# Kernel optimization log

Hardware: AMD Instinct MI355X
Metric: run time of the kernel (lower is better)

## Reference

```python
import jax, jax.numpy as jnp
import numpy as np

B, S, D, F, E, K = 2, 2048, 1024, 4096, 8, 2


def setup_inputs() -> dict:
    key = jax.random.key(0)
    ks = jax.random.split(key, 6)
    s = 0.02  # init scale
    return {
        "x": jax.random.normal(ks[0], (B, S, D), dtype=jnp.float32),
        "Wr": jax.random.normal(ks[1], (D, E), dtype=jnp.float32) * s,
        "br": jnp.zeros((E,), dtype=jnp.float32),
        "W1": jax.random.normal(ks[2], (E, D, F), dtype=jnp.float32) * s,
        "b1": jnp.zeros((E, F), dtype=jnp.float32),
        "W2": jax.random.normal(ks[3], (E, F, D), dtype=jnp.float32) * s,
        "b2": jnp.zeros((E, D), dtype=jnp.float32),
        "top_k": K,
    }


def reference(x, Wr, br, W1, b1, W2, b2, top_k):
    b, s, d = x.shape
    e = Wr.shape[1]
    xt = x.reshape(-1, d)                              # [T, D], T = b*s
    logits = xt @ Wr + br                              # [T, E]
    probs = jax.nn.softmax(logits, axis=-1)            # [T, E] router probabilities
    topw, topi = jax.lax.top_k(probs, top_k)           # [T, K] each
    # combine weight per (token, expert): weight if expert in token's top-k else 0
    cw = jnp.sum(jax.nn.one_hot(topi, e, dtype=x.dtype) * topw[..., None], axis=1)  # [T, E]
    # dense grouped FFN: every expert over every token, then weighted combine
    h = jax.nn.relu(jnp.einsum('td,edf->tef', xt, W1) + b1)   # [T, E, F]
    y = jnp.einsum('tef,efd->ted', h, W2) + b2                # [T, E, D]
    out = jnp.einsum('te,ted->td', cw, y).reshape(b, s, d)    # [B, S, D]
    return out, probs.reshape(b, s, e)
```

## Files before the change

### kernel.cpp

```cpp
#include <hip/hip_runtime.h>
#include <hip/hip_bf16.h>


#define T_TOK 4096
#define D_DIM 1024
#define F_DIM 4096
#define E_NUM 8
#define CAP_ROWS 10240
#define N_TILES (CAP_ROWS/256)

typedef __attribute__((ext_vector_type(8))) short short8v;
typedef __attribute__((ext_vector_type(8))) unsigned short ushort8v;
typedef __attribute__((ext_vector_type(4))) float f32x4;

static __device__ __forceinline__ unsigned short f2bf(float f){
  union { float f; unsigned u; } v; v.f = f;
  unsigned r = (v.u + 0x7fffu + ((v.u >> 16) & 1u)) >> 16;
  return (unsigned short)r;
}
static __device__ __forceinline__ float bf2f(unsigned short s){
  union { unsigned u; float f; } v; v.u = ((unsigned)s) << 16;
  return v.f;
}

static __device__ __forceinline__ void gload16(const void* g, void* l) {
  __builtin_amdgcn_global_load_lds(
      (const __attribute__((address_space(1))) unsigned int*)g,
      (__attribute__((address_space(3))) unsigned int*)l, 16, 0, 0);
}

__global__ __launch_bounds__(256) void k_init(int* counts, int* cursor,
                                              int* rows_token, float* rows_w){
  const int gid = blockIdx.x * 256 + threadIdx.x;
  if (gid < E_NUM) counts[gid] = 0;
  else if (gid < 2*E_NUM) cursor[gid - E_NUM] = 0;
  if (gid < CAP_ROWS) { rows_token[gid] = 0; rows_w[gid] = 0.f; }
}

__global__ __launch_bounds__(256) void k_router(
    const float* __restrict__ x, const float* __restrict__ Wr,
    const float* __restrict__ br, float* __restrict__ probs_out,
    int* __restrict__ topi, float* __restrict__ topw, int* __restrict__ counts,
    unsigned short* __restrict__ xbf)
{
  const int lane = threadIdx.x & 63;
  const int t = blockIdx.x * 4 + (threadIdx.x >> 6);
  float xv[16];
  #pragma unroll
  for (int i = 0; i < 16; ++i) xv[i] = x[(size_t)t*D_DIM + i*64 + lane];
  #pragma unroll
  for (int i = 0; i < 16; ++i) xbf[(size_t)t*D_DIM + i*64 + lane] = f2bf(xv[i]);
  float pe[E_NUM];
  #pragma unroll
  for (int e = 0; e < E_NUM; ++e) {
    float p = 0.f;
    #pragma unroll
    for (int i = 0; i < 16; ++i) p += xv[i] * Wr[(i*64 + lane)*E_NUM + e];
    #pragma unroll
    for (int off = 32; off >= 1; off >>= 1) p += __shfl_xor(p, off);
    pe[e] = p + br[e];
  }
  float m = pe[0];
  #pragma unroll
  for (int e = 1; e < E_NUM; ++e) m = fmaxf(m, pe[e]);
  float s = 0.f;
  #pragma unroll
  for (int e = 0; e < E_NUM; ++e) { pe[e] = expf(pe[e] - m); s += pe[e]; }
  const float inv = 1.f / s;
  int e1 = 0; float v1 = pe[0];
  #pragma unroll
  for (int e = 1; e < E_NUM; ++e) if (pe[e] > v1) { v1 = pe[e]; e1 = e; }
  int e2 = (e1 == 0) ? 1 : 0; float v2 = pe[e2];
  #pragma unroll
  for (int e = 0; e < E_NUM; ++e) if (e != e1 && pe[e] > v2) { v2 = pe[e]; e2 = e; }
  if (lane == 0) {
    #pragma unroll
    for (int e = 0; e < E_NUM; ++e) probs_out[(size_t)t*E_NUM + e] = pe[e] * inv;
    topi[t*2+0] = e1; topw[t*2+0] = v1 * inv;
    topi[t*2+1] = e2; topw[t*2+1] = v2 * inv;
    atomicAdd(&counts[e1], 1);
    atomicAdd(&counts[e2], 1);
  }
}

__global__ __launch_bounds__(256) void k_scan(
    const int* __restrict__ counts, int* __restrict__ pbase,
    int* __restrict__ tile_e)
{
  __shared__ int base_s[E_NUM + 1];
  const int tid = threadIdx.x;
  if (tid == 0) {
    int base = 0;
    #pragma unroll
    for (int e = 0; e < E_NUM; ++e) {
      base_s[e] = base;
      base += ((counts[e] + 255) >> 8) << 8;
    }
    base_s[E_NUM] = base;
  }
  __syncthreads();
  if (tid <= E_NUM) pbase[tid] = base_s[tid];
  if (tid < N_TILES) {
    const int r0 = tid << 8;
    int e = -1;
    #pragma unroll
    for (int k = 0; k < E_NUM; ++k)
      if (r0 >= base_s[k] && r0 < base_s[k+1]) e = k;
    tile_e[tid] = e;
  }
}

__global__ __launch_bounds__(256) void k_assign(
    const int* __restrict__ topi, const float* __restrict__ topw,
    const int* __restrict__ pbase, int* __restrict__ cursor,
    int* __restrict__ rows_token, float* __restrict__ rows_w,
    int* __restrict__ pair_of)
{
  const int t = blockIdx.x * 256 + threadIdx.x;
  if (t < T_TOK) {
    #pragma unroll
    for (int k = 0; k < 2; ++k) {
      const int e = topi[t*2+k];
      const int slot = atomicAdd(&cursor[e], 1);
      const int pid = pbase[e] + slot;
      rows_token[pid] = t;
      rows_w[pid] = topw[t*2+k];
      pair_of[t*2+k] = pid;
    }
  }
}

template<int R, int C>
__global__ __launch_bounds__(256) void k_tcvt(const float* __restrict__ in,
                                              unsigned short* __restrict__ out)
{
  const size_t eo = (size_t)blockIdx.z * R * C;
  const int r0 = blockIdx.y * 64, c0 = blockIdx.x * 64;
  __shared__ unsigned short ls[64][66];
  const int t = threadIdx.x;
  const int rr = t >> 4, cc = (t & 15) * 4;
  #pragma unroll
  for (int p = 0; p < 4; ++p) {
    const float4 v = *(const float4*)&in[eo + (size_t)(r0 + p*16 + rr)*C + c0 + cc];
    ls[p*16+rr][cc+0]=f2bf(v.x); ls[p*16+rr][cc+1]=f2bf(v.y);
    ls[p*16+rr][cc+2]=f2bf(v.z); ls[p*16+rr][cc+3]=f2bf(v.w);
  }
  __syncthreads();
  const int kc = (t & 7) * 8, nn0 = t >> 3;
  #pragma unroll
  for (int p = 0; p < 2; ++p) {
    const int nn = nn0 + p*32;
    ushort8v o;
    #pragma unroll
    for (int j = 0; j < 8; ++j) o[j] = ls[kc + j][nn];
    *(ushort8v*)&out[eo + (size_t)(c0 + nn)*R + r0 + kc] = o;
  }
}

template<bool GATHER, int NDIM, int KFULL, int EPI>
__global__ __launch_bounds__(512, 2) void k_gemm(
    const unsigned short* __restrict__ A,
    const unsigned short* __restrict__ Bt,
    const float* __restrict__ bias,
    const int* __restrict__ tile_e,
    const int* __restrict__ rows_token,
    const float* __restrict__ rows_w,
    unsigned short* __restrict__ outp,
    int nkt, int kch)
{
  const int tot = gridDim.x * gridDim.y;
  int flat = blockIdx.x * gridDim.y + blockIdx.y;
  flat = (flat & 7) * (tot >> 3) + (flat >> 3);
  const int bx = flat / gridDim.y;
  const int by = flat % gridDim.y;
  const int e = tile_e[by];
  if (e < 0) return;
  const int rt = by * 256;
  const int ntc = bx * 256;
  const int koff = blockIdx.z * kch;
  __shared__ __align__(16) unsigned short LB[3][512*32];
  const int tid = threadIdx.x;
  const int lane = tid & 63;
  const int w = tid >> 6;
  const int lrow = lane >> 2;
  const int g = (lane & 3) ^ (lrow & 3);
  const unsigned short* gp[4];
  unsigned lbase[4];
  if (w < 4) {
    #pragma unroll
    for (int i = 0; i < 4; ++i) {
      const int rl = w*64 + i*16 + lrow;
      const int rowidx = GATHER ? rows_token[rt + rl] : (rt + rl);
      gp[i] = A + (size_t)rowidx * KFULL + koff + g*8;
      lbase[i] = (unsigned)((w*64 + i*16) * 32);
    }
  } else {
    const unsigned short* Be = Bt + (size_t)e * NDIM * KFULL;
    #pragma unroll
    for (int i = 0; i < 4; ++i) {
      const int rl = (w-4)*64 + i*16 + lrow;
      gp[i] = Be + (size_t)(ntc + rl) * KFULL + koff + g*8;
      lbase[i] = (unsigned)((256 + (w-4)*64 + i*16) * 32);
    }
  }
  const int wr = w >> 2, wc = w & 3;
  const int cl = lane & 15, rgb = lane >> 4;
  const int ch = (rgb ^ (cl & 3)) * 8;
  f32x4 acc[8][4] = {};

  #define STG(tt, ss)                                  \
    { const int _ko = (tt) * 32;                       \
      gload16(gp[0] + _ko, &LB[ss][lbase[0]]);         \
      gload16(gp[1] + _ko, &LB[ss][lbase[1]]);         \
      gload16(gp[2] + _ko, &LB[ss][lbase[2]]);         \
      gload16(gp[3] + _ko, &LB[ss][lbase[3]]); }

  STG(0, 0)
  STG(1, 1)
  asm volatile("s_waitcnt vmcnt(4)" ::: "memory");
  __builtin_amdgcn_s_barrier();

  int cur = 0;
  for (int t = 0; t < nkt; ++t) {
    const int pb = (cur == 0) ? 2 : (cur - 1);
    if (t + 2 < nkt) STG(t+2, pb)
    const unsigned short* Sb = LB[cur];
    short8v a[8], b[4];
    #pragma unroll
    for (int m = 0; m < 8; ++m)
      a[m] = *(const short8v*)&Sb[(wr*128 + m*16 + cl)*32 + ch];
    #pragma unroll
    for (int n = 0; n < 4; ++n)
      b[n] = *(const short8v*)&Sb[(256 + wc*64 + n*16 + cl)*32 + ch];
    #pragma unroll
    for (int m = 0; m < 8; ++m)
      #pragma unroll
      for (int n = 0; n < 4; ++n)
        acc[m][n] = __builtin_amdgcn_mfma_f32_16x16x32_bf16(a[m], b[n], acc[m][n], 0, 0, 0);
    if (t + 2 < nkt) { asm volatile("s_waitcnt vmcnt(4)" ::: "memory"); }
    else             { asm volatile("s_waitcnt vmcnt(0)" ::: "memory"); }
    __builtin_amdgcn_s_barrier();
    cur = (cur == 2) ? 0 : (cur + 1);
  }
  #undef STG

  unsigned short* op = outp;
  if (EPI == 2) op += (size_t)blockIdx.z * CAP_ROWS * NDIM;
  const bool addb = (EPI == 1) || (blockIdx.z == 0);
  const size_t ebias = (size_t)e * NDIM;
  #pragma unroll
  for (int m = 0; m < 8; ++m) {
    const int row = rt + wr*128 + m*16 + rgb*4;
    float4 rw4 = make_float4(0,0,0,0);
    if (EPI == 2) rw4 = *(const float4*)&rows_w[row];
    #pragma unroll
    for (int n = 0; n < 4; ++n) {
      const int col = ntc + wc*64 + n*16 + cl;
      const float bv = addb ? bias[ebias + col] : 0.f;
      #pragma unroll
      for (int r = 0; r < 4; ++r) {
        float v = acc[m][n][r] + bv;
        if (EPI == 1) v = fmaxf(v, 0.f);
        else          v *= ((const float*)&rw4)[r];
        const unsigned short hb = f2bf(v);
        const unsigned short ob = (unsigned short)__shfl_xor((int)(unsigned)hb, 1);
        if ((lane & 1) == 0) {
          const unsigned pk = (unsigned)hb | ((unsigned)ob << 16);
          *(unsigned*)&op[(size_t)(row + r)*NDIM + col] = pk;
        }
      }
    }
  }
}

__global__ __launch_bounds__(256) void k_combine(
    const unsigned short* __restrict__ yp, const int* __restrict__ pair_of,
    float* __restrict__ out, int ksplit)
{
  const int gid = blockIdx.x * 256 + threadIdx.x;
  const int t = gid >> 7;
  const int c = (gid & 127) * 8;
  float o[8] = {0,0,0,0,0,0,0,0};
  #pragma unroll
  for (int k = 0; k < 2; ++k) {
    const int p = pair_of[t*2+k];
    for (int s = 0; s < ksplit; ++s) {
      const ushort8v v = *(const ushort8v*)&yp[((size_t)s*CAP_ROWS + p)*D_DIM + c];
      #pragma unroll
      for (int j = 0; j < 8; ++j) o[j] += bf2f(v[j]);
    }
  }
  float4 o0; o0.x=o[0]; o0.y=o[1]; o0.z=o[2]; o0.w=o[3];
  float4 o1; o1.x=o[4]; o1.y=o[5]; o1.z=o[6]; o1.w=o[7];
  *(float4*)&out[(size_t)t*D_DIM + c]     = o0;
  *(float4*)&out[(size_t)t*D_DIM + c + 4] = o1;
}

extern "C" void kernel_launch(void* const* d_in, const int* in_sizes, int n_in,
                              void* d_out, int out_size, void* d_ws, size_t ws_size,
                              hipStream_t stream)
{
  const float* x  = (const float*)d_in[0];
  const float* Wr = (const float*)d_in[1];
  const float* br = (const float*)d_in[2];
  const float* W1 = (const float*)d_in[3];
  const float* b1 = (const float*)d_in[4];
  const float* W2 = (const float*)d_in[5];
  const float* b2 = (const float*)d_in[6];
  (void)in_sizes; (void)n_in; (void)out_size;

  float* out   = (float*)d_out;
  float* probs = out + (size_t)T_TOK * D_DIM;

  char* w = (char*)d_ws;
  size_t off = 0;
  int*   counts     = (int*)(w + off); off += 256;
  int*   cursor     = (int*)(w + off); off += 256;
  int*   pbase      = (int*)(w + off); off += 512;
  int*   tile_e     = (int*)(w + off); off += 3072;
  int*   topi       = (int*)(w + off); off += (size_t)T_TOK*2*4;
  float* topw       = (float*)(w + off); off += (size_t)T_TOK*2*4;
  int*   pair_of    = (int*)(w + off); off += (size_t)T_TOK*2*4;
  int*   rows_token = (int*)(w + off); off += (size_t)CAP_ROWS*4;
  float* rows_w     = (float*)(w + off); off += (size_t)CAP_ROWS*4;
  off = (off + 255) & ~(size_t)255;
  unsigned short* xbf = (unsigned short*)(w + off); off += (size_t)T_TOK*D_DIM*2;
  unsigned short* Wt  = (unsigned short*)(w + off); off += (size_t)E_NUM*D_DIM*F_DIM*2;
  unsigned short* h   = (unsigned short*)(w + off); off += (size_t)CAP_ROWS*F_DIM*2;
  unsigned short* yp  = (unsigned short*)(w + off);
  const size_t ypart_bytes = (size_t)CAP_ROWS * D_DIM * 2;
  int ksplit = 1;
  if (ws_size >= off + 4 * ypart_bytes) ksplit = 4;
  else if (ws_size >= off + 2 * ypart_bytes) ksplit = 2;
  const int kch2 = F_DIM / ksplit;
  const int nkt2 = kch2 / 32;

  k_init<<<(CAP_ROWS + 255) / 256, 256, 0, stream>>>(counts, cursor, rows_token, rows_w);
  k_router<<<T_TOK / 4, 256, 0, stream>>>(x, Wr, br, probs, topi, topw, counts, xbf);
  k_scan<<<1, 256, 0, stream>>>(counts, pbase, tile_e);
  k_assign<<<T_TOK / 256, 256, 0, stream>>>(topi, topw, pbase, cursor,
                                            rows_token, rows_w, pair_of);
  k_tcvt<D_DIM, F_DIM><<<dim3(F_DIM/64, D_DIM/64, E_NUM), 256, 0, stream>>>(W1, Wt);
  k_gemm<true, F_DIM, D_DIM, 1><<<dim3(F_DIM/256, N_TILES, 1), 512, 0, stream>>>(
      xbf, Wt, b1, tile_e, rows_token, rows_w, h, D_DIM/32, D_DIM);
  k_tcvt<F_DIM, D_DIM><<<dim3(D_DIM/64, F_DIM/64, E_NUM), 256, 0, stream>>>(W2, Wt);
  k_gemm<false, D_DIM, F_DIM, 2><<<dim3(D_DIM/256, N_TILES, ksplit), 512, 0, stream>>>(
      h, Wt, b2, tile_e, rows_token, rows_w, yp, nkt2, kch2);
  k_combine<<<T_TOK * D_DIM / 8 / 256, 256, 0, stream>>>(yp, pair_of, out, ksplit);
}
```

Before: 475.1 us.

## Restructure grouped GEMM mainloop: BK=64 double buffer with interleaved LDS reads and MFMA

Replaces the triple-buffered BK=32 mainloop with a double-buffered BK=64 tile. Each iteration is split into four MFMA sub-blocks, and LDS fragment loads for the next sub-block are interleaved with the current one. Global staging is split into two halves, issued at different points in the iteration. The change also adds a new XOR swizzle over 8 chunks and uses s_setprio around the MFMA bursts. The aim is to halve loop/barrier overhead per K and to hide LDS and global latency behind math, at the cost of many more barriers per iteration and higher register pressure.

Result: faster. 464.2 us (-2.3%).

```diff
diff --git a/kernel.cpp b/kernel.cpp
--- a/kernel.cpp
+++ b/kernel.cpp
@@ -178,71 +178,129 @@
   const int rt = by * 256;
   const int ntc = bx * 256;
   const int koff = blockIdx.z * kch;
-  __shared__ __align__(16) unsigned short LB[3][512*32];
+  __shared__ __align__(16) unsigned short LB[2][512 * 64];
   const int tid = threadIdx.x;
   const int lane = tid & 63;
   const int w = tid >> 6;
-  const int lrow = lane >> 2;
-  const int g = (lane & 3) ^ (lrow & 3);
-  const unsigned short* gp[4];
-  unsigned lbase[4];
+  const int lr = lane >> 3;
+  const int g  = (lane & 7) ^ lr;
+  const unsigned short* gp[8];
+  unsigned lbase[8];
   if (w < 4) {
     #pragma unroll
-    for (int i = 0; i < 4; ++i) {
-      const int rl = w*64 + i*16 + lrow;
+    for (int i = 0; i < 8; ++i) {
+      const int rl = w*64 + i*8 + lr;
       const int rowidx = GATHER ? rows_token[rt + rl] : (rt + rl);
       gp[i] = A + (size_t)rowidx * KFULL + koff + g*8;
-      lbase[i] = (unsigned)((w*64 + i*16) * 32);
+      lbase[i] = (unsigned)((w*64 + i*8) * 64);
     }
   } else {
     const unsigned short* Be = Bt + (size_t)e * NDIM * KFULL;
     #pragma unroll
-    for (int i = 0; i < 4; ++i) {
-      const int rl = (w-4)*64 + i*16 + lrow;
+    for (int i = 0; i < 8; ++i) {
+      const int rl = (w-4)*64 + i*8 + lr;
       gp[i] = Be + (size_t)(ntc + rl) * KFULL + koff + g*8;
-      lbase[i] = (unsigned)((256 + (w-4)*64 + i*16) * 32);
+      lbase[i] = (unsigned)((256 + (w-4)*64 + i*8) * 64);
     }
   }
   const int wr = w >> 2, wc = w & 3;
   const int cl = lane & 15, rgb = lane >> 4;
-  const int ch = (rgb ^ (cl & 3)) * 8;
+  const int sz = cl & 7;
   f32x4 acc[8][4] = {};
 
-  #define STG(tt, ss)                                  \
-    { const int _ko = (tt) * 32;                       \
-      gload16(gp[0] + _ko, &LB[ss][lbase[0]]);         \
-      gload16(gp[1] + _ko, &LB[ss][lbase[1]]);         \
-      gload16(gp[2] + _ko, &LB[ss][lbase[2]]);         \
-      gload16(gp[3] + _ko, &LB[ss][lbase[3]]); }
-
-  STG(0, 0)
-  STG(1, 1)
+  #define STG4(tt, bb, c0)                                    \
+    { const int _ko = (tt) * 64;                              \
+      gload16(gp[c0+0] + _ko, &LB[bb][lbase[c0+0]]);          \
+      gload16(gp[c0+1] + _ko, &LB[bb][lbase[c0+1]]);          \
+      gload16(gp[c0+2] + _ko, &LB[bb][lbase[c0+2]]);          \
+      gload16(gp[c0+3] + _ko, &LB[bb][lbase[c0+3]]); }
+  #define LGK0  asm volatile("s_waitcnt lgkmcnt(0)" ::: "memory")
+  #define BAR   __builtin_amdgcn_s_barrier()
+
+  STG4(0, 0, 0) STG4(0, 0, 4)
+  STG4(1, 1, 0)
   asm volatile("s_waitcnt vmcnt(4)" ::: "memory");
-  __builtin_amdgcn_s_barrier();
-
-  int cur = 0;
+  BAR;
+
   for (int t = 0; t < nkt; ++t) {
-    const int pb = (cur == 0) ? 2 : (cur - 1);
-    if (t + 2 < nkt) STG(t+2, pb)
-    const unsigned short* Sb = LB[cur];
-    short8v a[8], b[4];
-    #pragma unroll
-    for (int m = 0; m < 8; ++m)
-      a[m] = *(const short8v*)&Sb[(wr*128 + m*16 + cl)*32 + ch];
-    #pragma unroll
-    for (int n = 0; n < 4; ++n)
-      b[n] = *(const short8v*)&Sb[(256 + wc*64 + n*16 + cl)*32 + ch];
-    #pragma unroll
-    for (int m = 0; m < 8; ++m)
-      #pragma unroll
-      for (int n = 0; n < 4; ++n)
-        acc[m][n] = __builtin_amdgcn_mfma_f32_16x16x32_bf16(a[m], b[n], acc[m][n], 0, 0, 0);
-    if (t + 2 < nkt) { asm volatile("s_waitcnt vmcnt(4)" ::: "memory"); }
-    else             { asm volatile("s_waitcnt vmcnt(0)" ::: "memory"); }
-    __builtin_amdgcn_s_barrier();
-    cur = (cur == 2) ? 0 : (cur + 1);
-  }
-  #undef STG
+    const int bb = t & 1;
+    const unsigned short* Sb = &LB[bb][0];
+    short8v a[4][2], b[4][2];
+    #pragma unroll
+    for (int m = 0; m < 4; ++m) {
+      a[m][0] = *(const short8v*)&Sb[(wr*128 + m*16 + cl)*64 + ((0*4+rgb)^sz)*8];
+      a[m][1] = *(const short8v*)&Sb[(wr*128 + m*16 + cl)*64 + ((1*4+rgb)^sz)*8];
+    }
+    #pragma unroll
+    for (int n = 0; n < 2; ++n) {
+      b[n][0] = *(const short8v*)&Sb[(256 + wc*64 + n*16 + cl)*64 + ((0*4+rgb)^sz)*8];
+      b[n][1] = *(const short8v*)&Sb[(256 + wc*64 + n*16 + cl)*64 + ((1*4+rgb)^sz)*8];
+    }
+    if (t + 1 < nkt) STG4(t+1, bb^1, 4)
+    BAR; LGK0;
+    __builtin_amdgcn_s_setprio(1);
+    #pragma unroll
+    for (int m = 0; m < 4; ++m)
+      #pragma unroll
+      for (int n = 0; n < 2; ++n) {
+        acc[m][n] = __builtin_amdgcn_mfma_f32_16x16x32_bf16(a[m][0], b[n][0], acc[m][n], 0, 0, 0);
+        acc[m][n] = __builtin_amdgcn_mfma_f32_16x16x32_bf16(a[m][1], b[n][1], acc[m][n], 0, 0, 0);
+      }
+    __builtin_amdgcn_s_setprio(0);
+    BAR;
+    #pragma unroll
+    for (int n = 2; n < 4; ++n) {
+      b[n][0] = *(const short8v*)&Sb[(256 + wc*64 + n*16 + cl)*64 + ((0*4+rgb)^sz)*8];
+      b[n][1] = *(const short8v*)&Sb[(256 + wc*64 + n*16 + cl)*64 + ((1*4+rgb)^sz)*8];
+    }
+    BAR; LGK0;
+    __builtin_amdgcn_s_setprio(1);
+    #pragma unroll
+    for (int m = 0; m < 4; ++m)
+      #pragma unroll
+      for (int n = 2; n < 4; ++n) {
+        acc[m][n] = __builtin_amdgcn_mfma_f32_16x16x32_bf16(a[m][0], b[n][0], acc[m][n], 0, 0, 0);
+        acc[m][n] = __builtin_amdgcn_mfma_f32_16x16x32_bf16(a[m][1], b[n][1], acc[m][n], 0, 0, 0);
+      }
+    __builtin_amdgcn_s_setprio(0);
+    BAR;
+    #pragma unroll
+    for (int m = 0; m < 4; ++m) {
+      a[m][0] = *(const short8v*)&Sb[(wr*128 + (m+4)*16 + cl)*64 + ((0*4+rgb)^sz)*8];
+      a[m][1] = *(const short8v*)&Sb[(wr*128 + (m+4)*16 + cl)*64 + ((1*4+rgb)^sz)*8];
+    }
+    BAR; LGK0;
+    __builtin_amdgcn_s_setprio(1);
+    #pragma unroll
+    for (int m = 0; m < 4; ++m)
+      #pragma unroll
+      for (int n = 0; n < 2; ++n) {
+        acc[m+4][n] = __builtin_amdgcn_mfma_f32_16x16x32_bf16(a[m][0], b[n][0], acc[m+4][n], 0, 0, 0);
+        acc[m+4][n] = __builtin_amdgcn_mfma_f32_16x16x32_bf16(a[m][1], b[n][1], acc[m+4][n], 0, 0, 0);
+      }
+    __builtin_amdgcn_s_setprio(0);
+    BAR;
+    if (t + 2 < nkt) {
+      STG4(t+2, bb, 0)
+      asm volatile("s_waitcnt vmcnt(4)" ::: "memory");
+    } else if (t + 1 < nkt) {
+      asm volatile("s_waitcnt vmcnt(0)" ::: "memory");
+    }
+    BAR;
+    __builtin_amdgcn_s_setprio(1);
+    #pragma unroll
+    for (int m = 0; m < 4; ++m)
+      #pragma unroll
+      for (int n = 2; n < 4; ++n) {
+        acc[m+4][n] = __builtin_amdgcn_mfma_f32_16x16x32_bf16(a[m][0], b[n][0], acc[m+4][n], 0, 0, 0);
+        acc[m+4][n] = __builtin_amdgcn_mfma_f32_16x16x32_bf16(a[m][1], b[n][1], acc[m+4][n], 0, 0, 0);
+      }
+    __builtin_amdgcn_s_setprio(0);
+    BAR;
+  }
+  #undef STG4
+  #undef LGK0
+  #undef BAR
 
   unsigned short* op = outp;
   if (EPI == 2) op += (size_t)blockIdx.z * CAP_ROWS * NDIM;
@@ -333,7 +391,7 @@
   if (ws_size >= off + 4 * ypart_bytes) ksplit = 4;
   else if (ws_size >= off + 2 * ypart_bytes) ksplit = 2;
   const int kch2 = F_DIM / ksplit;
-  const int nkt2 = kch2 / 32;
+  const int nkt2 = kch2 / 64;
 
   k_init<<<(CAP_ROWS + 255) / 256, 256, 0, stream>>>(counts, cursor, rows_token, rows_w);
   k_router<<<T_TOK / 4, 256, 0, stream>>>(x, Wr, br, probs, topi, topw, counts, xbf);
@@ -342,7 +400,7 @@
                                             rows_token, rows_w, pair_of);
   k_tcvt<D_DIM, F_DIM><<<dim3(F_DIM/64, D_DIM/64, E_NUM), 256, 0, stream>>>(W1, Wt);
   k_gemm<true, F_DIM, D_DIM, 1><<<dim3(F_DIM/256, N_TILES, 1), 512, 0, stream>>>(
-      xbf, Wt, b1, tile_e, rows_token, rows_w, h, D_DIM/32, D_DIM);
+      xbf, Wt, b1, tile_e, rows_token, rows_w, h, D_DIM/64, D_DIM);
   k_tcvt<F_DIM, D_DIM><<<dim3(D_DIM/64, F_DIM/64, E_NUM), 256, 0, stream>>>(W2, Wt);
   k_gemm<false, D_DIM, F_DIM, 2><<<dim3(D_DIM/256, N_TILES, ksplit), 512, 0, stream>>>(
       h, Wt, b2, tile_e, rows_token, rows_w, yp, nkt2, kch2);
```

## Shrink GEMM tiles to 128x128 with K=64 double buffering and merge routing kernels

Applied to the files above, without the earlier changes.

The grouped GEMMs move from 256x256 tiles with 512 threads and triple-buffered K=32 stages to 128x128 tiles with 256 threads, double-buffered K=64 stages, a new XOR swizzle and s_setprio around the MFMA block. Expert padding drops from 256 to 128 rows, which cuts wasted padded rows and lets capacity shrink to 9216. Scan and assign are fused into one kernel, and the init kernel becomes a memset. Smaller tiles reduce padding waste and add more blocks, but they lower per-block data reuse and the two-stage pipeline hides less load latency.

Result: no change. 469.3 us (-1.2%).

```diff
diff --git a/kernel.cpp b/kernel.cpp
--- a/kernel.cpp
+++ b/kernel.cpp
@@ -6,8 +6,8 @@
 #define D_DIM 1024
 #define F_DIM 4096
 #define E_NUM 8
-#define CAP_ROWS 10240
-#define N_TILES (CAP_ROWS/256)
+#define CAP_ROWS 9216
+#define N_TILES (CAP_ROWS/128)
 
 typedef __attribute__((ext_vector_type(8))) short short8v;
 typedef __attribute__((ext_vector_type(8))) unsigned short ushort8v;
@@ -27,14 +27,6 @@
   __builtin_amdgcn_global_load_lds(
       (const __attribute__((address_space(1))) unsigned int*)g,
       (__attribute__((address_space(3))) unsigned int*)l, 16, 0, 0);
-}
-
-__global__ __launch_bounds__(256) void k_init(int* counts, int* cursor,
-                                              int* rows_token, float* rows_w){
-  const int gid = blockIdx.x * 256 + threadIdx.x;
-  if (gid < E_NUM) counts[gid] = 0;
-  else if (gid < 2*E_NUM) cursor[gid - E_NUM] = 0;
-  if (gid < CAP_ROWS) { rows_token[gid] = 0; rows_w[gid] = 0.f; }
 }
 
 __global__ __launch_bounds__(256) void k_router(
@@ -83,46 +75,39 @@
   }
 }
 
-__global__ __launch_bounds__(256) void k_scan(
-    const int* __restrict__ counts, int* __restrict__ pbase,
-    int* __restrict__ tile_e)
+__global__ __launch_bounds__(256) void k_assign(
+    const int* __restrict__ counts,
+    const int* __restrict__ topi, const float* __restrict__ topw,
+    int* __restrict__ cursor,
+    int* __restrict__ rows_token, float* __restrict__ rows_w,
+    int* __restrict__ pair_of, int* __restrict__ tile_e)
 {
   __shared__ int base_s[E_NUM + 1];
-  const int tid = threadIdx.x;
-  if (tid == 0) {
+  if (threadIdx.x == 0) {
     int base = 0;
     #pragma unroll
     for (int e = 0; e < E_NUM; ++e) {
       base_s[e] = base;
-      base += ((counts[e] + 255) >> 8) << 8;
+      base += ((counts[e] + 127) >> 7) << 7;
     }
     base_s[E_NUM] = base;
   }
   __syncthreads();
-  if (tid <= E_NUM) pbase[tid] = base_s[tid];
-  if (tid < N_TILES) {
-    const int r0 = tid << 8;
+  if (blockIdx.x == 0 && threadIdx.x < N_TILES) {
+    const int r0 = threadIdx.x << 7;
     int e = -1;
     #pragma unroll
     for (int k = 0; k < E_NUM; ++k)
       if (r0 >= base_s[k] && r0 < base_s[k+1]) e = k;
-    tile_e[tid] = e;
-  }
-}
-
-__global__ __launch_bounds__(256) void k_assign(
-    const int* __restrict__ topi, const float* __restrict__ topw,
-    const int* __restrict__ pbase, int* __restrict__ cursor,
-    int* __restrict__ rows_token, float* __restrict__ rows_w,
-    int* __restrict__ pair_of)
-{
+    tile_e[threadIdx.x] = e;
+  }
   const int t = blockIdx.x * 256 + threadIdx.x;
   if (t < T_TOK) {
     #pragma unroll
     for (int k = 0; k < 2; ++k) {
       const int e = topi[t*2+k];
       const int slot = atomicAdd(&cursor[e], 1);
-      const int pid = pbase[e] + slot;
+      const int pid = base_s[e] + slot;
       rows_token[pid] = t;
       rows_w[pid] = topw[t*2+k];
       pair_of[t*2+k] = pid;
@@ -158,7 +143,7 @@
 }
 
 template<bool GATHER, int NDIM, int KFULL, int EPI>
-__global__ __launch_bounds__(512, 2) void k_gemm(
+__global__ __launch_bounds__(256, 2) void k_gemm(
     const unsigned short* __restrict__ A,
     const unsigned short* __restrict__ Bt,
     const float* __restrict__ bias,
@@ -175,82 +160,85 @@
   const int by = flat % gridDim.y;
   const int e = tile_e[by];
   if (e < 0) return;
-  const int rt = by * 256;
-  const int ntc = bx * 256;
+  const int rt = by * 128;
+  const int ntc = bx * 128;
   const int koff = blockIdx.z * kch;
-  __shared__ __align__(16) unsigned short LB[3][512*32];
+  __shared__ __align__(16) unsigned short LB[2][256 * 64];
   const int tid = threadIdx.x;
   const int lane = tid & 63;
   const int w = tid >> 6;
-  const int lrow = lane >> 2;
-  const int g = (lane & 3) ^ (lrow & 3);
-  const unsigned short* gp[4];
-  unsigned lbase[4];
-  if (w < 4) {
-    #pragma unroll
-    for (int i = 0; i < 4; ++i) {
-      const int rl = w*64 + i*16 + lrow;
+  const int lr = lane >> 3;
+  const int g  = (lane & 7) ^ lr;
+  const unsigned short* gp[8];
+  unsigned lbase[8];
+  if (w < 2) {
+    #pragma unroll
+    for (int i = 0; i < 8; ++i) {
+      const int rl = w*64 + i*8 + lr;
       const int rowidx = GATHER ? rows_token[rt + rl] : (rt + rl);
       gp[i] = A + (size_t)rowidx * KFULL + koff + g*8;
-      lbase[i] = (unsigned)((w*64 + i*16) * 32);
+      lbase[i] = (unsigned)((w*64 + i*8) * 64);
     }
   } else {
     const unsigned short* Be = Bt + (size_t)e * NDIM * KFULL;
     #pragma unroll
-    for (int i = 0; i < 4; ++i) {
-      const int rl = (w-4)*64 + i*16 + lrow;
+    for (int i = 0; i < 8; ++i) {
+      const int rl = (w-2)*64 + i*8 + lr;
       gp[i] = Be + (size_t)(ntc + rl) * KFULL + koff + g*8;
-      lbase[i] = (unsigned)((256 + (w-4)*64 + i*16) * 32);
-    }
-  }
-  const int wr = w >> 2, wc = w & 3;
+      lbase[i] = (unsigned)((128*64) + ((w-2)*64 + i*8) * 64);
+    }
+  }
+  const int wr = w >> 1, wc = w & 1;
   const int cl = lane & 15, rgb = lane >> 4;
-  const int ch = (rgb ^ (cl & 3)) * 8;
-  f32x4 acc[8][4] = {};
-
-  #define STG(tt, ss)                                  \
-    { const int _ko = (tt) * 32;                       \
-      gload16(gp[0] + _ko, &LB[ss][lbase[0]]);         \
-      gload16(gp[1] + _ko, &LB[ss][lbase[1]]);         \
-      gload16(gp[2] + _ko, &LB[ss][lbase[2]]);         \
-      gload16(gp[3] + _ko, &LB[ss][lbase[3]]); }
-
-  STG(0, 0)
-  STG(1, 1)
-  asm volatile("s_waitcnt vmcnt(4)" ::: "memory");
+  const int sz = cl & 7;
+  f32x4 acc[4][4] = {};
+
+  #define STG8(tt, bb)                                          \
+    { const int _ko = (tt) * 64;                                \
+      _Pragma("unroll")                                         \
+      for (int _i = 0; _i < 8; ++_i)                            \
+        gload16(gp[_i] + _ko, &LB[bb][lbase[_i]]); }
+
+  STG8(0, 0)
+  asm volatile("s_waitcnt vmcnt(0)" ::: "memory");
   __builtin_amdgcn_s_barrier();
 
-  int cur = 0;
   for (int t = 0; t < nkt; ++t) {
-    const int pb = (cur == 0) ? 2 : (cur - 1);
-    if (t + 2 < nkt) STG(t+2, pb)
-    const unsigned short* Sb = LB[cur];
-    short8v a[8], b[4];
-    #pragma unroll
-    for (int m = 0; m < 8; ++m)
-      a[m] = *(const short8v*)&Sb[(wr*128 + m*16 + cl)*32 + ch];
-    #pragma unroll
-    for (int n = 0; n < 4; ++n)
-      b[n] = *(const short8v*)&Sb[(256 + wc*64 + n*16 + cl)*32 + ch];
-    #pragma unroll
-    for (int m = 0; m < 8; ++m)
+    const int bb = t & 1;
+    if (t + 1 < nkt) STG8(t+1, bb^1)
+    const unsigned short* Sb = &LB[bb][0];
+    short8v a[4][2], b[4][2];
+    #pragma unroll
+    for (int m = 0; m < 4; ++m) {
+      a[m][0] = *(const short8v*)&Sb[(wr*64 + m*16 + cl)*64 + ((0*4+rgb)^sz)*8];
+      a[m][1] = *(const short8v*)&Sb[(wr*64 + m*16 + cl)*64 + ((1*4+rgb)^sz)*8];
+    }
+    #pragma unroll
+    for (int n = 0; n < 4; ++n) {
+      b[n][0] = *(const short8v*)&Sb[(128*64) + (wc*64 + n*16 + cl)*64 + ((0*4+rgb)^sz)*8];
+      b[n][1] = *(const short8v*)&Sb[(128*64) + (wc*64 + n*16 + cl)*64 + ((1*4+rgb)^sz)*8];
+    }
+    __builtin_amdgcn_s_setprio(1);
+    #pragma unroll
+    for (int m = 0; m < 4; ++m)
       #pragma unroll
-      for (int n = 0; n < 4; ++n)
-        acc[m][n] = __builtin_amdgcn_mfma_f32_16x16x32_bf16(a[m], b[n], acc[m][n], 0, 0, 0);
-    if (t + 2 < nkt) { asm volatile("s_waitcnt vmcnt(4)" ::: "memory"); }
-    else             { asm volatile("s_waitcnt vmcnt(0)" ::: "memory"); }
+      for (int n = 0; n < 4; ++n) {
+        acc[m][n] = __builtin_amdgcn_mfma_f32_16x16x32_bf16(a[m][0], b[n][0], acc[m][n], 0, 0, 0);
+        acc[m][n] = __builtin_amdgcn_mfma_f32_16x16x32_bf16(a[m][1], b[n][1], acc[m][n], 0, 0, 0);
+      }
+    __builtin_amdgcn_s_setprio(0);
+    asm volatile("s_waitcnt vmcnt(0)" ::: "memory");
     __builtin_amdgcn_s_barrier();
-    cur = (cur == 2) ? 0 : (cur + 1);
-  }
-  #undef STG
+  }
+  #undef STG8
 
   unsigned short* op = outp;
   if (EPI == 2) op += (size_t)blockIdx.z * CAP_ROWS * NDIM;
   const bool addb = (EPI == 1) || (blockIdx.z == 0);
   const size_t ebias = (size_t)e * NDIM;
   #pragma unroll
-  for (int m = 0; m < 8; ++m) {
-    const int row = rt + wr*128 + m*16 + rgb*4;
+  for (int m = 0; m < 4; ++m) {
+    const int row = rt + wr*64 + m*16 + rgb*4;
     float4 rw4 = make_float4(0,0,0,0);
     if (EPI == 2) rw4 = *(const float4*)&rows_w[row];
     #pragma unroll
@@ -316,13 +304,13 @@
   size_t off = 0;
   int*   counts     = (int*)(w + off); off += 256;
   int*   cursor     = (int*)(w + off); off += 256;
-  int*   pbase      = (int*)(w + off); off += 512;
+  int*   rows_token = (int*)(w + off); off += (size_t)CAP_ROWS*4;
+  float* rows_w     = (float*)(w + off); off += (size_t)CAP_ROWS*4;
+  const size_t zbytes = off;
   int*   tile_e     = (int*)(w + off); off += 3072;
   int*   topi       = (int*)(w + off); off += (size_t)T_TOK*2*4;
   float* topw       = (float*)(w + off); off += (size_t)T_TOK*2*4;
   int*   pair_of    = (int*)(w + off); off += (size_t)T_TOK*2*4;
-  int*   rows_token = (int*)(w + off); off += (size_t)CAP_ROWS*4;
-  float* rows_w     = (float*)(w + off); off += (size_t)CAP_ROWS*4;
   off = (off + 255) & ~(size_t)255;
   unsigned short* xbf = (unsigned short*)(w + off); off += (size_t)T_TOK*D_DIM*2;
   unsigned short* Wt  = (unsigned short*)(w + off); off += (size_t)E_NUM*D_DIM*F_DIM*2;
@@ -333,18 +321,17 @@
   if (ws_size >= off + 4 * ypart_bytes) ksplit = 4;
   else if (ws_size >= off + 2 * ypart_bytes) ksplit = 2;
   const int kch2 = F_DIM / ksplit;
-  const int nkt2 = kch2 / 32;
-
-  k_init<<<(CAP_ROWS + 255) / 256, 256, 0, stream>>>(counts, cursor, rows_token, rows_w);
+  const int nkt2 = kch2 / 64;
+
+  hipMemsetAsync(d_ws, 0, zbytes, stream);
   k_router<<<T_TOK / 4, 256, 0, stream>>>(x, Wr, br, probs, topi, topw, counts, xbf);
-  k_scan<<<1, 256, 0, stream>>>(counts, pbase, tile_e);
-  k_assign<<<T_TOK / 256, 256, 0, stream>>>(topi, topw, pbase, cursor,
-                                            rows_token, rows_w, pair_of);
+  k_assign<<<T_TOK / 256, 256, 0, stream>>>(counts, topi, topw, cursor,
+                                            rows_token, rows_w, pair_of, tile_e);
   k_tcvt<D_DIM, F_DIM><<<dim3(F_DIM/64, D_DIM/64, E_NUM), 256, 0, stream>>>(W1, Wt);
-  k_gemm<true, F_DIM, D_DIM, 1><<<dim3(F_DIM/256, N_TILES, 1), 512, 0, stream>>>(
-      xbf, Wt, b1, tile_e, rows_token, rows_w, h, D_DIM/32, D_DIM);
+  k_gemm<true, F_DIM, D_DIM, 1><<<dim3(F_DIM/128, N_TILES, 1), 256, 0, stream>>>(
+      xbf, Wt, b1, tile_e, rows_token, rows_w, h, D_DIM/64, D_DIM);
   k_tcvt<F_DIM, D_DIM><<<dim3(D_DIM/64, F_DIM/64, E_NUM), 256, 0, stream>>>(W2, Wt);
-  k_gemm<false, D_DIM, F_DIM, 2><<<dim3(D_DIM/256, N_TILES, ksplit), 512, 0, stream>>>(
+  k_gemm<false, D_DIM, F_DIM, 2><<<dim3(D_DIM/128, N_TILES, ksplit), 256, 0, stream>>>(
       h, Wt, b2, tile_e, rows_token, rows_w, yp, nkt2, kch2);
   k_combine<<<T_TOK * D_DIM / 8 / 256, 256, 0, stream>>>(yp, pair_of, out, ksplit);
 }
```
